# Optimization experiments

Hardware: AMD Instinct MI355X
Metric: run time of the kernel (lower is better)

Reference implementation:

```python
import jax, jax.numpy as jnp
import numpy as np

GROUP_SIZES = [16, 16, 16, 16]
K = 2
TEMPERATURE = 1.0
NEG = float(np.finfo(np.float32).min)  # torch.finfo(dtype).min


def setup_inputs() -> dict:
    key = jax.random.key(0)
    k1, k2, k3 = jax.random.split(key, 3)
    B, S, D, E, G = 8, 4096, 1024, 64, len(GROUP_SIZES)
    x = jax.random.normal(k1, (B, S, D), dtype=jnp.float32)
    W_group = jax.random.normal(k2, (G, D), dtype=jnp.float32) * 0.02
    W_expert = jax.random.normal(k3, (E, D), dtype=jnp.float32) * 0.02
    return {"x": x, "W_group": W_group, "W_expert": W_expert}


def reference(x, W_group, W_expert):
    E = W_expert.shape[0]
    # group id of each expert (contiguous ranges) -- static
    expert_group = jnp.asarray(np.repeat(np.arange(len(GROUP_SIZES)), GROUP_SIZES))  # [E]

    # gate logits (no bias), temperature scaling
    expert_logits = jnp.einsum('bsd,ed->bse', x, W_expert) * (1.0 / TEMPERATURE)  # [B,S,E]
    group_logits = jnp.einsum('bsd,gd->bsg', x, W_group)                          # [B,S,G]
    group_probs = jax.nn.softmax(group_logits, axis=-1)
    g_idx = jnp.argmax(group_probs, axis=-1)                                      # [B,S]

    # mask experts outside the selected group's contiguous range
    mask = expert_group[None, None, :] != g_idx[..., None]                        # [B,S,E] bool
    mdt = mask.astype(expert_logits.dtype)
    masked_logits = mdt * NEG + (1.0 - mdt) * expert_logits

    probs_full = jax.nn.softmax(masked_logits, axis=-1)                           # [B,S,E]
    topk_vals, idx = jax.lax.top_k(masked_logits, K)                              # [B,S,K]
    scores = jax.nn.softmax(topk_vals, axis=-1)

    # aux stats (no_grad in original)
    importance = jax.lax.stop_gradient(jnp.mean(probs_full, axis=(0, 1)))         # [E]
    counts = jnp.zeros((E,), probs_full.dtype).at[idx.reshape(-1)].add(1.0)       # [E]
    load = counts / jnp.maximum(jnp.sum(counts), 1.0)
    return (idx, scores, probs_full, importance, load)
```

## Files before the change

kernel.cpp:

```cpp
#include <hip/hip_runtime.h>
#include <math.h>

#define TOKENS   32768
#define DDIM     1024
#define TPB      64
#define NBLOCKS  (TOKENS / TPB)

#define OFF_SCORES 65536
#define OFF_PROBS  131072
#define OFF_IMP    2228224
#define OFF_LOAD   2228288

#define NSLOT 16

typedef __attribute__((ext_vector_type(8))) short  short8;
typedef __attribute__((ext_vector_type(4))) float  f32x4;
typedef __attribute__((ext_vector_type(4))) int    intx4;

__device__ __attribute__((aligned(16))) short wfrag[32 * 5 * 3 * 64 * 8];

__device__ inline unsigned rne_hi(float x) {
  unsigned u = __float_as_uint(x);
  unsigned r = u + 0x7fffu + ((u >> 16) & 1u);
  return r & 0xffff0000u;
}

__device__ inline void split3(const float* xv, short8& f1, short8& f2, short8& f3) {
  int o1[4], o2[4], o3[4];
  #pragma unroll
  for (int p = 0; p < 4; ++p) {
    float x0 = xv[2*p], x1 = xv[2*p+1];
    unsigned h0 = rne_hi(x0), h1 = rne_hi(x1);
    o1[p] = (int)((h0 >> 16) | (h1 & 0xffff0000u));
    float r0 = x0 - __uint_as_float(h0);
    float r1 = x1 - __uint_as_float(h1);
    unsigned g0 = rne_hi(r0), g1 = rne_hi(r1);
    o2[p] = (int)((g0 >> 16) | (g1 & 0xffff0000u));
    float s0 = r0 - __uint_as_float(g0);
    float s1 = r1 - __uint_as_float(g1);
    unsigned w0 = rne_hi(s0), w1 = rne_hi(s1);
    o3[p] = (int)((w0 >> 16) | (w1 & 0xffff0000u));
  }
  intx4 t1 = {o1[0], o1[1], o1[2], o1[3]};
  intx4 t2 = {o2[0], o2[1], o2[2], o2[3]};
  intx4 t3 = {o3[0], o3[1], o3[2], o3[3]};
  f1 = __builtin_bit_cast(short8, t1);
  f2 = __builtin_bit_cast(short8, t2);
  f3 = __builtin_bit_cast(short8, t3);
}

__global__ void prep_kernel(const float* __restrict__ Wg, const float* __restrict__ We) {
  const int nt   = blockIdx.x >> 5;
  const int ks   = blockIdx.x & 31;
  const int lane = threadIdx.x & 63;
  const int row  = nt * 16 + (lane & 15);
  const int k0   = ks * 32 + (lane >> 4) * 8;
  float xv[8];
  #pragma unroll
  for (int j = 0; j < 8; ++j) {
    float v = 0.f;
    if (row < 64)      v = We[(size_t)row * DDIM + k0 + j];
    else if (row < 68) v = Wg[(size_t)(row - 64) * DDIM + k0 + j];
    xv[j] = v;
  }
  short8 f1, f2, f3;
  split3(xv, f1, f2, f3);
  short8* dst = (short8*)wfrag + (((size_t)ks * 5 + nt) * 3) * 64 + lane;
  dst[0]   = f1;
  dst[64]  = f2;
  dst[128] = f3;
}

__global__ __launch_bounds__(256)
__attribute__((amdgpu_waves_per_eu(2)))
void router_kernel(const float* __restrict__ x,
                   float* __restrict__ out,
                   float* __restrict__ ws) {
  __shared__ __attribute__((aligned(16))) float el[TPB * 88];
  __shared__ __attribute__((aligned(16))) short8 bstage[30 * 64];
  __shared__ int cnt[64];
  const int tid    = threadIdx.x;
  const int lane   = tid & 63;
  const int wv     = tid >> 6;
  const int khalf  = wv >> 1;
  const int mhalf  = wv & 1;
  const int quad   = lane >> 4;
  const int m      = lane & 15;
  const int tokblk = blockIdx.x * TPB;

  if (tid < 64) cnt[tid] = 0;

  const float* apb = x + (size_t)(tokblk + mhalf * 32 + m) * DDIM + khalf * 512 + quad * 8;
  const short8* wsrc = (const short8*)wfrag;

  f32x4 ahi[2][5], alo[2][5];
  #pragma unroll
  for (int mt = 0; mt < 2; ++mt)
    #pragma unroll
    for (int nt = 0; nt < 5; ++nt) { ahi[mt][nt] = 0.f; alo[mt][nt] = 0.f; }

  float4 cur[4], nxt[4];
  #pragma unroll
  for (int mt = 0; mt < 2; ++mt) {
    const float* p = apb + (size_t)(mt * 16) * DDIM;
    cur[mt * 2]     = *(const float4*)(p);
    cur[mt * 2 + 1] = *(const float4*)(p + 4);
  }

  short8 breg[8];
  #pragma unroll
  for (int j = 0; j < 8; ++j) {
    const int c = wv + 4 * j;
    if (c < 30) {
      const int ksg = (c < 15) ? 0 : 16;
      const int fr  = (c < 15) ? c : c - 15;
      breg[j] = wsrc[((size_t)ksg * 15 + fr) * 64 + lane];
    }
  }
  #pragma unroll
  for (int j = 0; j < 8; ++j) {
    const int c = wv + 4 * j;
    if (c < 30) bstage[c * 64 + lane] = breg[j];
  }
  __syncthreads();

  for (int ks = 0; ks < 16; ++ks) {
    short8 fb[5][3];
    #pragma unroll
    for (int nt = 0; nt < 5; ++nt) {
      const short8* bp = &bstage[(khalf * 15 + nt * 3) * 64 + lane];
      fb[nt][0] = bp[0];
      fb[nt][1] = bp[64];
      fb[nt][2] = bp[128];
    }
    if (ks < 15) {
      #pragma unroll
      for (int j = 0; j < 8; ++j) {
        const int c = wv + 4 * j;
        if (c < 30) {
          const int ksg = (c < 15) ? (ks + 1) : (16 + ks + 1);
          const int fr  = (c < 15) ? c : c - 15;
          breg[j] = wsrc[((size_t)ksg * 15 + fr) * 64 + lane];
        }
      }
    }
    const int kpf = (ks + 1 < 16) ? (ks + 1) : 15;
    #pragma unroll
    for (int mt = 0; mt < 2; ++mt) {
      const float* p = apb + (size_t)(mt * 16) * DDIM + kpf * 32;
      nxt[mt * 2]     = *(const float4*)(p);
      nxt[mt * 2 + 1] = *(const float4*)(p + 4);
    }
    #pragma unroll
    for (int mt = 0; mt < 2; ++mt) {
      float av[8] = {cur[mt*2].x, cur[mt*2].y, cur[mt*2].z, cur[mt*2].w,
                     cur[mt*2+1].x, cur[mt*2+1].y, cur[mt*2+1].z, cur[mt*2+1].w};
      short8 fa0, fa1, fa2;
      split3(av, fa0, fa1, fa2);
      #pragma unroll
      for (int nt = 0; nt < 5; ++nt) {
        ahi[mt][nt] = __builtin_amdgcn_mfma_f32_16x16x32_bf16(fa0, fb[nt][0], ahi[mt][nt], 0, 0, 0);
        f32x4 c = alo[mt][nt];
        c = __builtin_amdgcn_mfma_f32_16x16x32_bf16(fa0, fb[nt][1], c, 0, 0, 0);
        c = __builtin_amdgcn_mfma_f32_16x16x32_bf16(fa1, fb[nt][0], c, 0, 0, 0);
        c = __builtin_amdgcn_mfma_f32_16x16x32_bf16(fa1, fb[nt][1], c, 0, 0, 0);
        c = __builtin_amdgcn_mfma_f32_16x16x32_bf16(fa0, fb[nt][2], c, 0, 0, 0);
        c = __builtin_amdgcn_mfma_f32_16x16x32_bf16(fa2, fb[nt][0], c, 0, 0, 0);
        c = __builtin_amdgcn_mfma_f32_16x16x32_bf16(fa1, fb[nt][2], c, 0, 0, 0);
        c = __builtin_amdgcn_mfma_f32_16x16x32_bf16(fa2, fb[nt][1], c, 0, 0, 0);
        alo[mt][nt] = c;
      }
    }
    #pragma unroll
    for (int i = 0; i < 4; ++i) cur[i] = nxt[i];
    if (ks < 15) {
      __syncthreads();
      #pragma unroll
      for (int j = 0; j < 8; ++j) {
        const int c = wv + 4 * j;
        if (c < 30) bstage[c * 64 + lane] = breg[j];
      }
      __syncthreads();
    }
  }

  if (khalf == 1) {
    #pragma unroll
    for (int mt = 0; mt < 2; ++mt)
      #pragma unroll
      for (int nt = 0; nt < 5; ++nt)
        #pragma unroll
        for (int r = 0; r < 4; ++r)
          el[(mhalf * 32 + mt * 16 + quad * 4 + r) * 88 + nt * 16 + m] = ahi[mt][nt][r] + alo[mt][nt][r];
  }
  __syncthreads();
  if (khalf == 0) {
    #pragma unroll
    for (int mt = 0; mt < 2; ++mt)
      #pragma unroll
      for (int nt = 0; nt < 5; ++nt)
        #pragma unroll
        for (int r = 0; r < 4; ++r) {
          const int idx = (mhalf * 32 + mt * 16 + quad * 4 + r) * 88 + nt * 16 + m;
          el[idx] += ahi[mt][nt][r] + alo[mt][nt][r];
        }
  }
  __syncthreads();

  if (tid < TPB) {
    const int t = tid;
    float* row = el + t * 88;
    const float g0 = row[64], g1 = row[65], g2 = row[66], g3 = row[67];
    int g = 0; float gb = g0;
    if (g1 > gb) { g = 1; gb = g1; }
    if (g2 > gb) { g = 2; gb = g2; }
    if (g3 > gb) { g = 3; gb = g3; }
    const int base = g << 4;
    float l[16];
    #pragma unroll
    for (int e = 0; e < 16; ++e) l[e] = row[base + e];
    int i1 = 0; float v1 = l[0];
    #pragma unroll
    for (int e = 1; e < 16; ++e) if (l[e] > v1) { i1 = e; v1 = l[e]; }
    int i2 = -1; float v2 = 0.f;
    #pragma unroll
    for (int e = 0; e < 16; ++e) {
      if (e == i1) continue;
      if (i2 < 0 || l[e] > v2) { i2 = e; v2 = l[e]; }
    }
    float pr[16]; float s = 0.f;
    #pragma unroll
    for (int e = 0; e < 16; ++e) { pr[e] = expf(l[e] - v1); s += pr[e]; }
    const float inv = 1.f / s;
    #pragma unroll
    for (int c = 0; c < 64; ++c) row[c] = 0.f;
    #pragma unroll
    for (int e = 0; e < 16; ++e) row[base + e] = pr[e] * inv;
    const size_t T = (size_t)tokblk + t;
    out[2*T]     = (float)(base + i1);
    out[2*T + 1] = (float)(base + i2);
    const float e2 = expf(v2 - v1);
    const float si = 1.f / (1.f + e2);
    out[OFF_SCORES + 2*T]     = si;
    out[OFF_SCORES + 2*T + 1] = e2 * si;
    atomicAdd(&cnt[base + i1], 1);
    atomicAdd(&cnt[base + i2], 1);
  }
  __syncthreads();

  for (int i = tid; i < TPB * 64; i += 256) {
    const int t = i >> 6, c = i & 63;
    out[OFF_PROBS + (((size_t)(tokblk + t)) << 6) + c] = el[t * 88 + c];
  }
  if (tid < 64) {
    const int e = tid;
    float s = 0.f;
    #pragma unroll 4
    for (int t = 0; t < TPB; ++t) s += el[t * 88 + e];
    const int slot = (blockIdx.x & (NSLOT - 1)) * 128;
    atomicAdd(&ws[slot + e], s);
    atomicAdd(&ws[slot + 64 + e], (float)cnt[e]);
  }
}

__global__ void finalize_kernel(const float* __restrict__ ws, float* __restrict__ out) {
  const int e = threadIdx.x;
  if (e < 64) {
    float imp = 0.f, cf = 0.f;
    #pragma unroll
    for (int s = 0; s < NSLOT; ++s) {
      imp += ws[s * 128 + e];
      cf  += ws[s * 128 + 64 + e];
    }
    out[OFF_IMP  + e] = imp * (1.0f / 32768.0f);
    out[OFF_LOAD + e] = cf  * (1.0f / 65536.0f);
  }
}

extern "C" void kernel_launch(void* const* d_in, const int* in_sizes, int n_in,
                              void* d_out, int out_size, void* d_ws, size_t ws_size,
                              hipStream_t stream) {
  (void)in_sizes; (void)n_in; (void)out_size; (void)ws_size;
  const float* x  = (const float*)d_in[0];
  const float* Wg = (const float*)d_in[1];
  const float* We = (const float*)d_in[2];
  float* out = (float*)d_out;
  float* ws  = (float*)d_ws;
  hipMemsetAsync(d_ws, 0, NSLOT * 128 * sizeof(float), stream);
  hipLaunchKernelGGL(prep_kernel, dim3(160), dim3(64), 0, stream, Wg, We);
  hipLaunchKernelGGL(router_kernel, dim3(NBLOCKS), dim3(256), 0, stream, x, out, ws);
  hipLaunchKernelGGL(finalize_kernel, dim3(1), dim3(64), 0, stream, ws, out);
}
```

Baseline: 208.4 us.

## Double-buffer weight fragments in LDS and interleave fragment loads with MFMAs

Weight fragments are staged in two alternating LDS buffers, which removes one barrier per k-step. The B fragments are loaded one n-tile ahead while the MFMAs run, with the loop order swapped so both m-tiles share each fragment. The el and bstage arrays now alias one shared-memory region, and the workspace memset is folded into prep_kernel to save an API call. LDS use per block grows, which could limit occupancy.

```diff
diff --git a/kernel.cpp b/kernel.cpp
--- a/kernel.cpp
+++ b/kernel.cpp
@@ -49,10 +49,12 @@
   f3 = __builtin_bit_cast(short8, t3);
 }
 
-__global__ void prep_kernel(const float* __restrict__ Wg, const float* __restrict__ We) {
+__global__ void prep_kernel(const float* __restrict__ Wg, const float* __restrict__ We,
+                            float* __restrict__ ws) {
   const int nt   = blockIdx.x >> 5;
   const int ks   = blockIdx.x & 31;
   const int lane = threadIdx.x & 63;
+  if (blockIdx.x < 32) ws[blockIdx.x * 64 + lane] = 0.f;
   const int row  = nt * 16 + (lane & 15);
   const int k0   = ks * 32 + (lane >> 4) * 8;
   float xv[8];
@@ -76,9 +78,10 @@
 void router_kernel(const float* __restrict__ x,
                    float* __restrict__ out,
                    float* __restrict__ ws) {
-  __shared__ __attribute__((aligned(16))) float el[TPB * 88];
-  __shared__ __attribute__((aligned(16))) short8 bstage[30 * 64];
-  __shared__ int cnt[64];
+  __shared__ __attribute__((aligned(16))) char smem[61440 + 256];
+  float*  el     = (float*)smem;
+  short8* bstage = (short8*)smem;
+  int*    cnt    = (int*)(smem + 61440);
   const int tid    = threadIdx.x;
   const int lane   = tid & 63;
   const int wv     = tid >> 6;
@@ -107,32 +110,28 @@
     cur[mt * 2 + 1] = *(const float4*)(p + 4);
   }
 
-  short8 breg[8];
-  #pragma unroll
-  for (int j = 0; j < 8; ++j) {
-    const int c = wv + 4 * j;
-    if (c < 30) {
-      const int ksg = (c < 15) ? 0 : 16;
-      const int fr  = (c < 15) ? c : c - 15;
-      breg[j] = wsrc[((size_t)ksg * 15 + fr) * 64 + lane];
-    }
-  }
-  #pragma unroll
-  for (int j = 0; j < 8; ++j) {
-    const int c = wv + 4 * j;
-    if (c < 30) bstage[c * 64 + lane] = breg[j];
+  {
+    short8 breg[8];
+    #pragma unroll
+    for (int j = 0; j < 8; ++j) {
+      const int c = wv + 4 * j;
+      if (c < 30) {
+        const int ksg = (c < 15) ? 0 : 16;
+        const int fr  = (c < 15) ? c : c - 15;
+        breg[j] = wsrc[((size_t)ksg * 15 + fr) * 64 + lane];
+      }
+    }
+    #pragma unroll
+    for (int j = 0; j < 8; ++j) {
+      const int c = wv + 4 * j;
+      if (c < 30) bstage[c * 64 + lane] = breg[j];
+    }
   }
   __syncthreads();
 
   for (int ks = 0; ks < 16; ++ks) {
-    short8 fb[5][3];
-    #pragma unroll
-    for (int nt = 0; nt < 5; ++nt) {
-      const short8* bp = &bstage[(khalf * 15 + nt * 3) * 64 + lane];
-      fb[nt][0] = bp[0];
-      fb[nt][1] = bp[64];
-      fb[nt][2] = bp[128];
-    }
+    const int pb = ks & 1;
+    short8 breg[8];
     if (ks < 15) {
       #pragma unroll
       for (int j = 0; j < 8; ++j) {
@@ -151,37 +150,48 @@
       nxt[mt * 2]     = *(const float4*)(p);
       nxt[mt * 2 + 1] = *(const float4*)(p + 4);
     }
+    short8 fa[2][3];
     #pragma unroll
     for (int mt = 0; mt < 2; ++mt) {
       float av[8] = {cur[mt*2].x, cur[mt*2].y, cur[mt*2].z, cur[mt*2].w,
                      cur[mt*2+1].x, cur[mt*2+1].y, cur[mt*2+1].z, cur[mt*2+1].w};
-      short8 fa0, fa1, fa2;
-      split3(av, fa0, fa1, fa2);
-      #pragma unroll
-      for (int nt = 0; nt < 5; ++nt) {
-        ahi[mt][nt] = __builtin_amdgcn_mfma_f32_16x16x32_bf16(fa0, fb[nt][0], ahi[mt][nt], 0, 0, 0);
+      split3(av, fa[mt][0], fa[mt][1], fa[mt][2]);
+    }
+    const short8* bbase = &bstage[(size_t)pb * 1920 + (size_t)khalf * 15 * 64 + lane];
+    short8 fb0 = bbase[0], fb1 = bbase[64], fb2 = bbase[128];
+    #pragma unroll
+    for (int nt = 0; nt < 5; ++nt) {
+      short8 n0, n1, n2;
+      if (nt < 4) {
+        n0 = bbase[(nt + 1) * 192];
+        n1 = bbase[(nt + 1) * 192 + 64];
+        n2 = bbase[(nt + 1) * 192 + 128];
+      }
+      #pragma unroll
+      for (int mt = 0; mt < 2; ++mt) {
+        ahi[mt][nt] = __builtin_amdgcn_mfma_f32_16x16x32_bf16(fa[mt][0], fb0, ahi[mt][nt], 0, 0, 0);
         f32x4 c = alo[mt][nt];
-        c = __builtin_amdgcn_mfma_f32_16x16x32_bf16(fa0, fb[nt][1], c, 0, 0, 0);
-        c = __builtin_amdgcn_mfma_f32_16x16x32_bf16(fa1, fb[nt][0], c, 0, 0, 0);
-        c = __builtin_amdgcn_mfma_f32_16x16x32_bf16(fa1, fb[nt][1], c, 0, 0, 0);
-        c = __builtin_amdgcn_mfma_f32_16x16x32_bf16(fa0, fb[nt][2], c, 0, 0, 0);
-        c = __builtin_amdgcn_mfma_f32_16x16x32_bf16(fa2, fb[nt][0], c, 0, 0, 0);
-        c = __builtin_amdgcn_mfma_f32_16x16x32_bf16(fa1, fb[nt][2], c, 0, 0, 0);
-        c = __builtin_amdgcn_mfma_f32_16x16x32_bf16(fa2, fb[nt][1], c, 0, 0, 0);
+        c = __builtin_amdgcn_mfma_f32_16x16x32_bf16(fa[mt][0], fb1, c, 0, 0, 0);
+        c = __builtin_amdgcn_mfma_f32_16x16x32_bf16(fa[mt][1], fb0, c, 0, 0, 0);
+        c = __builtin_amdgcn_mfma_f32_16x16x32_bf16(fa[mt][1], fb1, c, 0, 0, 0);
+        c = __builtin_amdgcn_mfma_f32_16x16x32_bf16(fa[mt][0], fb2, c, 0, 0, 0);
+        c = __builtin_amdgcn_mfma_f32_16x16x32_bf16(fa[mt][2], fb0, c, 0, 0, 0);
+        c = __builtin_amdgcn_mfma_f32_16x16x32_bf16(fa[mt][1], fb2, c, 0, 0, 0);
+        c = __builtin_amdgcn_mfma_f32_16x16x32_bf16(fa[mt][2], fb1, c, 0, 0, 0);
         alo[mt][nt] = c;
       }
-    }
-    #pragma unroll
-    for (int i = 0; i < 4; ++i) cur[i] = nxt[i];
+      if (nt < 4) { fb0 = n0; fb1 = n1; fb2 = n2; }
+    }
     if (ks < 15) {
-      __syncthreads();
       #pragma unroll
       for (int j = 0; j < 8; ++j) {
         const int c = wv + 4 * j;
-        if (c < 30) bstage[c * 64 + lane] = breg[j];
+        if (c < 30) bstage[(size_t)(pb ^ 1) * 1920 + c * 64 + lane] = breg[j];
       }
       __syncthreads();
     }
+    #pragma unroll
+    for (int i = 0; i < 4; ++i) cur[i] = nxt[i];
   }
 
   if (khalf == 1) {
@@ -286,8 +296,7 @@
   const float* We = (const float*)d_in[2];
   float* out = (float*)d_out;
   float* ws  = (float*)d_ws;
-  hipMemsetAsync(d_ws, 0, NSLOT * 128 * sizeof(float), stream);
-  hipLaunchKernelGGL(prep_kernel, dim3(160), dim3(64), 0, stream, Wg, We);
+  hipLaunchKernelGGL(prep_kernel, dim3(160), dim3(64), 0, stream, Wg, We, ws);
   hipLaunchKernelGGL(router_kernel, dim3(NBLOCKS), dim3(256), 0, stream, x, out, ws);
   hipLaunchKernelGGL(finalize_kernel, dim3(1), dim3(64), 0, stream, ws, out);
 }
```

Result: no change. 206.5 us (median of 2 runs) (-0.9%).
